# Performance work log

Hardware: AMD Instinct MI355X
Metric: run time of the kernel (lower is better)

## Reference

```python
import jax, jax.numpy as jnp
import numpy as np

GRID_SIZE = 5   # efficient-kan default
K = 3           # spline_order
BATCH = 32768
OBS_DIM = 128
ACTION_DIM = 18
# (in_features, out_features) for the 7 KANLinear layers:
# base: 128->256->256->64 ; adv head: 64->64->18 ; value head: 64->64->1
DIMS = [(OBS_DIM, 256), (256, 256), (256, 64), (64, 64), (64, ACTION_DIM), (64, 64), (64, 1)]


def make_grid(in_f):
    # uniform grid on [-1,1] extended by K knots each side: shape (in_f, GRID_SIZE+2K+1)
    h = 2.0 / GRID_SIZE
    g = jnp.arange(-K, GRID_SIZE + K + 1, dtype=jnp.float32) * h - 1.0
    return jnp.broadcast_to(g, (in_f, g.shape[0]))


def b_splines(x, grid):
    # Cox-de Boor recursion; x: (B, in) -> bases (B, in, GRID_SIZE+K)
    xe = x[:, :, None]
    b = ((xe >= grid[:, :-1]) & (xe < grid[:, 1:])).astype(x.dtype)
    for j in range(1, K + 1):
        left = (xe - grid[:, : -(j + 1)]) / (grid[:, j:-1] - grid[:, : -(j + 1)])
        right = (grid[:, j + 1:] - xe) / (grid[:, j + 1:] - grid[:, 1:-j])
        b = left * b[:, :, :-1] + right * b[:, :, 1:]
    return b


def kan_layer(x, bw, sw, sc):
    # efficient-kan KANLinear: silu base path + spline path with standalone scaler
    grid = make_grid(x.shape[1])
    base = jax.nn.silu(x) @ bw.T                              # (B, out)
    bases = b_splines(x, grid)                                # (B, in, G+K)
    spline = jnp.einsum('big,oig->bo', bases, sw * sc[:, :, None])
    return base + spline


def setup_inputs() -> dict:
    key = jax.random.key(0)
    ks = jax.random.split(key, 1 + 3 * len(DIMS))
    inp = {"x": jax.random.normal(ks[0], (BATCH, OBS_DIM), dtype=jnp.float32)}
    for i, (fin, fout) in enumerate(DIMS):
        inp[f"bw{i}"] = jax.random.normal(ks[1 + 3 * i], (fout, fin), dtype=jnp.float32) / np.sqrt(fin).astype(np.float32)
        inp[f"sw{i}"] = jax.random.normal(ks[2 + 3 * i], (fout, fin, GRID_SIZE + K), dtype=jnp.float32) * (0.1 / np.sqrt(fin).astype(np.float32))
        inp[f"sc{i}"] = 1.0 + 0.1 * jax.random.normal(ks[3 + 3 * i], (fout, fin), dtype=jnp.float32)
    return inp


def reference(x, bw0, sw0, sc0, bw1, sw1, sc1, bw2, sw2, sc2,
              bw3, sw3, sc3, bw4, sw4, sc4, bw5, sw5, sc5, bw6, sw6, sc6):
    h = x
    for bw, sw, sc in [(bw0, sw0, sc0), (bw1, sw1, sc1), (bw2, sw2, sc2)]:
        h = kan_layer(h, bw, sw, sc)
    advantage = kan_layer(kan_layer(h, bw3, sw3, sc3), bw4, sw4, sc4)
    state_value = kan_layer(kan_layer(h, bw5, sw5, sc5), bw6, sw6, sc6)
    return (advantage, state_value)
```

## Files before the change

### kernel.cpp

```cpp
#include <hip/hip_runtime.h>

typedef unsigned short u16;
typedef unsigned int   u32;
typedef unsigned long long u64;
typedef __bf16 bf16;
typedef float f32x4  __attribute__((ext_vector_type(4)));
typedef bf16  bf16x8 __attribute__((ext_vector_type(8)));

__device__ __forceinline__ float bf2f(u16 u){ return (float)__builtin_bit_cast(bf16,u); }
__device__ __forceinline__ u16   f2bf(float f){ return __builtin_bit_cast(u16,(bf16)f); }
__device__ __forceinline__ u32   pkbf(float a,float b){ return (u32)f2bf(a)|((u32)f2bf(b)<<16); }

#define NROWS 32768

__device__ __forceinline__ uint4 basis_pk(float x)
{
  float tp  = __fmaf_rn(x, 2.5f, 5.5f);
  float tpc = fminf(fmaxf(tp, -1.0f), 12.0f);
  float fi  = floorf(tpc);
  float uu  = tpc - fi;
  int   i0  = (int)fi;
  float u2 = uu*uu, u3 = u2*uu, w1 = 1.0f-uu, w2 = w1*w1, w3 = w2*w1;
  float d1 = __fmaf_rn(3.0f, u3, __fmaf_rn(-6.0f, u2, 4.0f));
  float d2 = __fmaf_rn(3.0f, w3, __fmaf_rn(-6.0f, w2, 4.0f));
  u64 dpk = (u64)pkbf(w3, d1) | ((u64)pkbf(d2, u3) << 32);
  int ss = i0*16 - 48;
  u64 A  = dpk << (ss & 63);
  u64 Bv = dpk >> ((64-ss) & 63);
  u64 Cv = dpk << ((ss-64) & 63);
  u64 Dv = dpk >> ((-ss) & 63);
  u64 lo = (ss>=0 && ss<64)   ? A  : ((ss<0 && ss>-64) ? Dv : 0ull);
  u64 hi = (ss>=64 && ss<128) ? Cv : ((ss>0 && ss<64)  ? Bv : 0ull);
  uint4 r; r.x=(u32)lo; r.y=(u32)(lo>>32); r.z=(u32)hi; r.w=(u32)(hi>>32);
  return r;
}

__device__ __forceinline__ void expand9(float x, u16& sil, uint4& bpk)
{
  float s = x * (1.0f/(1.0f+__expf(-x)));
  sil = f2bf(s);
  bpk = basis_pk(x);
}
__device__ __forceinline__ void expand10(float x, u32& spk, uint4& bpk)
{
  float s = x * (1.0f/(1.0f+__expf(-x)));
  u16 uh = f2bf(s);
  u16 ul = f2bf(s - bf2f(uh));
  spk = (u32)uh | ((u32)ul<<16);
  bpk = basis_pk(x);
}

struct PrepArgs {
  const float* bw[7]; const float* sw[7]; const float* sc[7];
  u16* w[7];
  int cin[7]; int coutr[7]; int ntsh[7]; int fmt[7];
  u32 elems[7];
};

__global__ __launch_bounds__(256) void prep_kernel(PrepArgs pa)
{
  u32 idx = blockIdx.x*256 + threadIdx.x;
  int L = 0;
  u32 off = idx;
  while (L < 6 && off >= pa.elems[L]) { off -= pa.elems[L]; ++L; }
  int j    = off & 7;
  int lane = (off>>3) & 63;
  u32 tl   = off >> 9;
  int ntsh = pa.ntsh[L];
  u32 kstep = tl >> ntsh;
  int ntile = (int)(tl & ((1u<<ntsh)-1u));
  int o    = ntile*16 + (lane&15);
  int kpos = (lane>>4)*8 + j;
  int i = 0, g = 0; bool sil;
  if (pa.fmt[L] == 0){
    u32 c = kstep/9u; int r = (int)(kstep - c*9u);
    if (r == 0){ i = (int)c*32 + kpos; sil = true; }
    else { int kl=(r-1)*32+kpos; i=(int)c*32+(kl>>3); g=kl&7; sil = false; }
  } else {
    u32 c = kstep/5u; int r = (int)(kstep - c*5u);
    if (r == 0){ i = (int)c*16 + (kpos>>1); sil = true; }
    else { int kl=(r-1)*32+kpos; i=(int)c*16+(kl>>3); g=kl&7; sil = false; }
  }
  float v = 0.f;
  if (o < pa.coutr[L]) {
    size_t e = (size_t)o*pa.cin[L] + i;
    v = sil ? pa.bw[L][e] : pa.sw[L][e*8+g]*pa.sc[L][e]*0.16666666666666666f;
  }
  pa.w[L][off] = f2bf(v);
}

template<int CIN,int COUT,int IN_MODE,int OUT_MODE>
__global__ __launch_bounds__(512,4) void kan_layer(const void* __restrict__ hin_,
    const u16* __restrict__ W, void* __restrict__ hout_)
{
  constexpr int NCH = CIN/32;
  constexpr int TOTK = NCH*9;
  constexpr int NTILES = COUT/16;
  constexpr int NT = (COUT>=128)? COUT/128 : 1;
  constexpr int SROW=20, BROW=132, BOFF=64*SROW;
  constexpr int CHUNK = BOFF + 64*BROW;
  __shared__ u32 buf[2][CHUNK];

  const int b0 = blockIdx.x*64;
  const int tid = threadIdx.x;
  const int wave = tid>>6, lane = tid&63, m = lane&15, quad = lane>>4;

  const u16*   __restrict__ hb = (const u16*)hin_;
  const float* __restrict__ hf = (const float*)hin_;

  f32x4 acc[4][NT];
#pragma unroll
  for (int a=0;a<4;++a)
#pragma unroll
    for (int n=0;n<NT;++n) acc[a][n]=(f32x4){0.f,0.f,0.f,0.f};

  bf16x8 bbuf[3][NT];
  auto loadB = [&](int kstep, bf16x8* dst){
    if (kstep < TOTK){
#pragma unroll
      for (int nt=0; nt<NT; ++nt)
        dst[nt] = *(const bf16x8*)(W + (((size_t)kstep*NTILES + ((wave*NT+nt)&(NTILES-1)))*64 + lane)*8);
    }
  };
  loadB(0, bbuf[0]); loadB(1, bbuf[1]);

  float xb[2][4];
  auto loadX = [&](int kc, float* dst){
#pragma unroll
    for (int t=0;t<4;++t){
      int task = t*512+tid, row = task>>5, f = task&31;
      int gi = (b0+row)*CIN + kc*32 + f;
      dst[t] = (IN_MODE==0)? hf[gi] : bf2f(hb[gi]);
    }
  };
  auto expandChunk = [&](const float* xc, u32* dstb){
#pragma unroll
    for (int t=0;t<4;++t){
      int task=t*512+tid, row=task>>5, f=task&31;
      u16 sil; uint4 bpk;
      expand9(xc[t], sil, bpk);
      ((u16*)dstb)[row*(SROW*2) + f] = sil;
      *(uint4*)&dstb[BOFF + row*BROW + f*4] = bpk;
    }
  };

  loadX(0, xb[0]);
  expandChunk(xb[0], buf[0]);
  if (NCH > 1) loadX(1, xb[1]);
  __syncthreads();

  for (int kc=0; kc<NCH; ++kc){
    u32* cur = buf[kc&1];
    u32* nxt = buf[(kc+1)&1];
    if (kc+1 < NCH) expandChunk(xb[(kc+1)&1], nxt);
    if (kc+2 < NCH) loadX(kc+2, xb[kc&1]);
#pragma unroll
    for (int ks=0; ks<9; ++ks){
      const int kstep = kc*9 + ks;
      loadB(kstep+2, bbuf[2]);
      bf16x8 af[4];
#pragma unroll
      for (int mt=0; mt<4; ++mt){
        int row = mt*16 + m;
        af[mt] = (ks==0)
          ? *(const bf16x8*)&cur[row*SROW + quad*4]
          : *(const bf16x8*)&cur[BOFF + row*BROW + (ks-1)*16 + quad*4];
      }
#pragma unroll
      for (int nt=0; nt<NT; ++nt)
#pragma unroll
        for (int mt=0; mt<4; ++mt)
          acc[mt][nt] = __builtin_amdgcn_mfma_f32_16x16x32_bf16(af[mt], bbuf[0][nt], acc[mt][nt],0,0,0);
#pragma unroll
      for (int nt=0; nt<NT; ++nt){ bbuf[0][nt]=bbuf[1][nt]; bbuf[1][nt]=bbuf[2][nt]; }
    }
    __syncthreads();
  }

  if (wave*NT < NTILES){
#pragma unroll
    for (int mt=0; mt<4; ++mt)
#pragma unroll
      for (int nt=0; nt<NT; ++nt)
#pragma unroll
        for (int r=0; r<4; ++r){
          size_t off = (size_t)(b0 + mt*16 + quad*4 + r)*COUT + ((wave*NT+nt)&(NTILES-1))*16 + m;
          if constexpr (OUT_MODE==0) ((float*)hout_)[off] = acc[mt][nt][r];
          else                       ((u16*)hout_)[off]   = f2bf(acc[mt][nt][r]);
        }
  }
}

template<int IN_MODE>
__global__ __launch_bounds__(512,4) void tail_kernel(const void* __restrict__ h2_,
  const u16* __restrict__ W3, const u16* __restrict__ W4,
  const u16* __restrict__ W5, const u16* __restrict__ W6,
  float* __restrict__ out_adv, float* __restrict__ out_val)
{
  constexpr int SROW=20, BROW=68, BOFF=64*20;
  __shared__ u32   Aexp[BOFF + 64*BROW];
  __shared__ float hA[64*65], hV[64*65];

  const int b0 = blockIdx.x*64;
  const int tid = threadIdx.x;
  const int wave = tid>>6, lane = tid&63, m = lane&15, quad = lane>>4;
  const int rg = wave>>2, cg = wave&3;

  const u16*   __restrict__ hb = (const u16*)h2_;
  const float* __restrict__ hf = (const float*)h2_;

  f32x4 a3[2], a5[2];
#pragma unroll
  for (int mt=0;mt<2;++mt){ a3[mt]=(f32x4){0,0,0,0}; a5[mt]=(f32x4){0,0,0,0}; }

  bf16x8 w3b[3], w5b[3];
  auto loadB2 = [&](int kstep, int d){
    if (kstep < 20){
      size_t bi = (((size_t)kstep*4 + cg)*64 + lane)*8;
      w3b[d] = *(const bf16x8*)(W3+bi);
      w5b[d] = *(const bf16x8*)(W5+bi);
    }
  };
  loadB2(0,0); loadB2(1,1);

  float xb[2][2];
  auto loadX = [&](int kc, float* dst){
#pragma unroll
    for (int t=0;t<2;++t){
      int task = t*512+tid, row=task>>4, f=task&15;
      int gi = (b0+row)*64 + kc*16 + f;
      dst[t] = (IN_MODE==0)? hf[gi] : bf2f(hb[gi]);
    }
  };
  loadX(0, xb[0]);

  for (int kc=0; kc<4; ++kc){
    const float* xc = xb[kc&1];
#pragma unroll
    for (int t=0;t<2;++t){
      int task=t*512+tid, row=task>>4, f=task&15;
      u32 spk; uint4 bpk;
      expand10(xc[t], spk, bpk);
      Aexp[row*SROW + f] = spk;
      *(uint4*)&Aexp[BOFF + row*BROW + f*4] = bpk;
    }
    if (kc+1 < 4) loadX(kc+1, xb[(kc+1)&1]);
    __syncthreads();
#pragma unroll
    for (int ks=0; ks<5; ++ks){
      const int kstep = kc*5 + ks;
      loadB2(kstep+2, 2);
      bf16x8 af[2];
#pragma unroll
      for (int mt=0; mt<2; ++mt){
        int row = rg*32 + mt*16 + m;
        af[mt] = (ks==0)
          ? *(const bf16x8*)&Aexp[row*SROW + quad*4]
          : *(const bf16x8*)&Aexp[BOFF + row*BROW + (ks-1)*16 + quad*4];
      }
#pragma unroll
      for (int mt=0; mt<2; ++mt){
        a3[mt] = __builtin_amdgcn_mfma_f32_16x16x32_bf16(af[mt], w3b[0], a3[mt],0,0,0);
        a5[mt] = __builtin_amdgcn_mfma_f32_16x16x32_bf16(af[mt], w5b[0], a5[mt],0,0,0);
      }
      w3b[0]=w3b[1]; w3b[1]=w3b[2]; w5b[0]=w5b[1]; w5b[1]=w5b[2];
    }
    __syncthreads();
  }
#pragma unroll
  for (int mt=0;mt<2;++mt)
#pragma unroll
    for (int r=0;r<4;++r){
      int row = rg*32 + mt*16 + quad*4 + r;
      hA[row*65 + cg*16 + m] = a3[mt][r];
      hV[row*65 + cg*16 + m] = a5[mt][r];
    }
  __syncthreads();

  f32x4 a4[2];
#pragma unroll
  for (int mt=0;mt<2;++mt) a4[mt]=(f32x4){0,0,0,0};
  bf16x8 w4b[3];
  auto loadB4 = [&](int kstep, int d){
    if (kstep < 20) w4b[d] = *(const bf16x8*)(W4 + (((size_t)kstep*4 + cg)*64 + lane)*8);
  };
  loadB4(0,0); loadB4(1,1);
  for (int kc=0; kc<4; ++kc){
#pragma unroll
    for (int t=0;t<2;++t){
      int task=t*512+tid, row=task>>4, f=task&15;
      u32 spk; uint4 bpk;
      expand10(hA[row*65 + kc*16 + f], spk, bpk);
      Aexp[row*SROW + f] = spk;
      *(uint4*)&Aexp[BOFF + row*BROW + f*4] = bpk;
    }
    __syncthreads();
#pragma unroll
    for (int ks=0; ks<5; ++ks){
      loadB4(kc*5+ks+2, 2);
      bf16x8 af[2];
#pragma unroll
      for (int mt=0; mt<2; ++mt){
        int row = rg*32 + mt*16 + m;
        af[mt] = (ks==0)
          ? *(const bf16x8*)&Aexp[row*SROW + quad*4]
          : *(const bf16x8*)&Aexp[BOFF + row*BROW + (ks-1)*16 + quad*4];
      }
#pragma unroll
      for (int mt=0; mt<2; ++mt)
        a4[mt] = __builtin_amdgcn_mfma_f32_16x16x32_bf16(af[mt], w4b[0], a4[mt],0,0,0);
      w4b[0]=w4b[1]; w4b[1]=w4b[2];
    }
    __syncthreads();
  }
  {
    int col = cg*16 + m;
    if (col < 18){
#pragma unroll
      for (int mt=0;mt<2;++mt)
#pragma unroll
        for (int r=0;r<4;++r)
          out_adv[(size_t)(b0 + rg*32 + mt*16 + quad*4 + r)*18 + col] = a4[mt][r];
    }
  }

  f32x4 a6[2];
#pragma unroll
  for (int mt=0;mt<2;++mt) a6[mt]=(f32x4){0,0,0,0};
  bf16x8 w6b[3];
  auto loadB6 = [&](int kstep, int d){
    if (kstep < 20) w6b[d] = *(const bf16x8*)(W6 + (((size_t)kstep*4 + cg)*64 + lane)*8);
  };
  loadB6(0,0); loadB6(1,1);
  for (int kc=0; kc<4; ++kc){
#pragma unroll
    for (int t=0;t<2;++t){
      int task=t*512+tid, row=task>>4, f=task&15;
      u32 spk; uint4 bpk;
      expand10(hV[row*65 + kc*16 + f], spk, bpk);
      Aexp[row*SROW + f] = spk;
      *(uint4*)&Aexp[BOFF + row*BROW + f*4] = bpk;
    }
    __syncthreads();
#pragma unroll
    for (int ks=0; ks<5; ++ks){
      loadB6(kc*5+ks+2, 2);
      bf16x8 af[2];
#pragma unroll
      for (int mt=0; mt<2; ++mt){
        int row = rg*32 + mt*16 + m;
        af[mt] = (ks==0)
          ? *(const bf16x8*)&Aexp[row*SROW + quad*4]
          : *(const bf16x8*)&Aexp[BOFF + row*BROW + (ks-1)*16 + quad*4];
      }
#pragma unroll
      for (int mt=0; mt<2; ++mt)
        a6[mt] = __builtin_amdgcn_mfma_f32_16x16x32_bf16(af[mt], w6b[0], a6[mt],0,0,0);
      w6b[0]=w6b[1]; w6b[1]=w6b[2];
    }
    __syncthreads();
  }
  if (cg==0 && m==0){
#pragma unroll
    for (int mt=0;mt<2;++mt)
#pragma unroll
      for (int r=0;r<4;++r)
        out_val[b0 + rg*32 + mt*16 + quad*4 + r] = a6[mt][r];
  }
}

extern "C" void kernel_launch(void* const* d_in, const int* in_sizes, int n_in,
                              void* d_out, int out_size, void* d_ws, size_t ws_size,
                              hipStream_t stream)
{
  (void)in_sizes; (void)n_in; (void)out_size;
  char* ws = (char*)d_ws;

  const size_t wbytes[7] = {589824u, 1179648u, 294912u, 81920u, 81920u, 81920u, 81920u};
  const bool midf32 = ws_size >= 77889536u;

  u16* W[7];
  char *h0, *h1, *h2;
  if (midf32) {
    h0 = ws;
    h1 = h0 + 33554432u;
    h2 = h1 + 33554432u;
    size_t off = 75497472u;
    for (int l=0;l<7;++l){ W[l] = (u16*)(ws+off); off += wbytes[l]; }
  } else {
    h0 = ws;
    h1 = h0 + 16777216u;
    h2 = h1 + 16777216u;
    size_t off = 37748736u;
    for (int l=0;l<7;++l){ W[l] = (u16*)(ws+off); off += wbytes[l]; }
  }

  PrepArgs pa;
  const int cins[7]   = {128,256,256,64,64,64,64};
  const int coutr[7]  = {256,256,64,64,18,64,1};
  const int ntsh[7]   = {4,4,2,2,2,2,2};
  const int fmts[7]   = {0,0,0,1,1,1,1};
  const u32 elems[7]  = {294912u,589824u,147456u,40960u,40960u,40960u,40960u};
  for (int l=0;l<7;++l){
    pa.bw[l] = (const float*)d_in[1+3*l];
    pa.sw[l] = (const float*)d_in[2+3*l];
    pa.sc[l] = (const float*)d_in[3+3*l];
    pa.w[l]  = W[l];
    pa.cin[l]=cins[l]; pa.coutr[l]=coutr[l]; pa.ntsh[l]=ntsh[l]; pa.fmt[l]=fmts[l];
    pa.elems[l]=elems[l];
  }
  prep_kernel<<<4672, 256, 0, stream>>>(pa);

  dim3 g(NROWS/64), b(512);
  float* out_adv = (float*)d_out;
  float* out_val = (float*)d_out + (size_t)NROWS*18;
  if (midf32) {
    kan_layer<128,256,0,0><<<g,b,0,stream>>>(d_in[0], W[0], h0);
    kan_layer<256,256,0,0><<<g,b,0,stream>>>(h0, W[1], h1);
    kan_layer<256, 64,0,0><<<g,b,0,stream>>>(h1, W[2], h2);
    tail_kernel<0><<<g,b,0,stream>>>(h2, W[3], W[4], W[5], W[6], out_adv, out_val);
  } else {
    kan_layer<128,256,0,1><<<g,b,0,stream>>>(d_in[0], W[0], h0);
    kan_layer<256,256,1,1><<<g,b,0,stream>>>(h0, W[1], h1);
    kan_layer<256, 64,1,1><<<g,b,0,stream>>>(h1, W[2], h2);
    tail_kernel<1><<<g,b,0,stream>>>(h2, W[3], W[4], W[5], W[6], out_adv, out_val);
  }
}
```

Baseline: 231.1 us.

## Switch main KAN layers to 32x32x16 MFMA tiles with 256-thread blocks

Rewrites the three main KAN layer kernels to use 32x32x16 bf16 MFMA instructions instead of 16x16x32. Blocks shrink to 4 waves, each computing a larger output fragment, with K-chunks of 16 input features and a deeper B prefetch. The prep kernel repacks the weight layout to match. This aims to reduce LDS A-fragment reads and instruction count per FLOP, at the cost of fewer waves per block, higher register pressure and a changed LDS layout.

Result: slower. 246.9 us (+6.8%).

```diff
diff --git a/kernel.cpp b/kernel.cpp
--- a/kernel.cpp
+++ b/kernel.cpp
@@ -4,8 +4,9 @@
 typedef unsigned int   u32;
 typedef unsigned long long u64;
 typedef __bf16 bf16;
-typedef float f32x4  __attribute__((ext_vector_type(4)));
-typedef bf16  bf16x8 __attribute__((ext_vector_type(8)));
+typedef float f32x4   __attribute__((ext_vector_type(4)));
+typedef float f32x16  __attribute__((ext_vector_type(16)));
+typedef bf16  bf16x8  __attribute__((ext_vector_type(8)));
 
 __device__ __forceinline__ float bf2f(u16 u){ return (float)__builtin_bit_cast(bf16,u); }
 __device__ __forceinline__ u16   f2bf(float f){ return __builtin_bit_cast(u16,(bf16)f); }
@@ -68,15 +69,17 @@
   u32 tl   = off >> 9;
   int ntsh = pa.ntsh[L];
   u32 kstep = tl >> ntsh;
-  int ntile = (int)(tl & ((1u<<ntsh)-1u));
-  int o    = ntile*16 + (lane&15);
-  int kpos = (lane>>4)*8 + j;
-  int i = 0, g = 0; bool sil;
+  int nt   = (int)(tl & ((1u<<ntsh)-1u));
+  int i = 0, g = 0, o; bool sil;
   if (pa.fmt[L] == 0){
+    o = nt*32 + (lane&31);
+    int koct = lane>>5;
     u32 c = kstep/9u; int r = (int)(kstep - c*9u);
-    if (r == 0){ i = (int)c*32 + kpos; sil = true; }
-    else { int kl=(r-1)*32+kpos; i=(int)c*32+(kl>>3); g=kl&7; sil = false; }
+    if (r == 0){ i = (int)c*16 + koct*8 + j; sil = true; }
+    else       { i = (int)c*16 + (r-1)*2 + koct; g = j; sil = false; }
   } else {
+    o = nt*16 + (lane&15);
+    int kpos = (lane>>4)*8 + j;
     u32 c = kstep/5u; int r = (int)(kstep - c*5u);
     if (r == 0){ i = (int)c*16 + (kpos>>1); sil = true; }
     else { int kl=(r-1)*32+kpos; i=(int)c*16+(kl>>3); g=kl&7; sil = false; }
@@ -90,53 +93,58 @@
 }
 
 template<int CIN,int COUT,int IN_MODE,int OUT_MODE>
-__global__ __launch_bounds__(512,4) void kan_layer(const void* __restrict__ hin_,
+__global__ __launch_bounds__(256,2) void kan_layer(const void* __restrict__ hin_,
     const u16* __restrict__ W, void* __restrict__ hout_)
 {
-  constexpr int NCH = CIN/32;
+  constexpr int NCH  = CIN/16;
   constexpr int TOTK = NCH*9;
-  constexpr int NTILES = COUT/16;
-  constexpr int NT = (COUT>=128)? COUT/128 : 1;
-  constexpr int SROW=20, BROW=132, BOFF=64*SROW;
+  constexpr int NT32 = COUT/32;
+  constexpr int RFW  = (COUT>=128)?2:1;
+  constexpr int CFW  = (COUT>=128)?COUT/128:1;
+  constexpr int SROW=12, BROW=68, BOFF=64*SROW;
   constexpr int CHUNK = BOFF + 64*BROW;
   __shared__ u32 buf[2][CHUNK];
 
   const int b0 = blockIdx.x*64;
   const int tid = threadIdx.x;
-  const int wave = tid>>6, lane = tid&63, m = lane&15, quad = lane>>4;
+  const int wave = tid>>6, lane = tid&63, m32 = lane&31, koct = lane>>5;
+  const int rfbase = (COUT>=128)? 0 : (wave>>1);
+  const int cfb    = (COUT>=128)? wave*CFW : (wave&1);
 
   const u16*   __restrict__ hb = (const u16*)hin_;
   const float* __restrict__ hf = (const float*)hin_;
 
-  f32x4 acc[4][NT];
-#pragma unroll
-  for (int a=0;a<4;++a)
-#pragma unroll
-    for (int n=0;n<NT;++n) acc[a][n]=(f32x4){0.f,0.f,0.f,0.f};
-
-  bf16x8 bbuf[3][NT];
+  f32x16 acc[RFW][CFW];
+#pragma unroll
+  for (int a=0;a<RFW;++a)
+#pragma unroll
+    for (int c=0;c<CFW;++c)
+#pragma unroll
+      for (int e=0;e<16;++e) acc[a][c][e] = 0.f;
+
+  bf16x8 bbuf[4][CFW];
   auto loadB = [&](int kstep, bf16x8* dst){
     if (kstep < TOTK){
 #pragma unroll
-      for (int nt=0; nt<NT; ++nt)
-        dst[nt] = *(const bf16x8*)(W + (((size_t)kstep*NTILES + ((wave*NT+nt)&(NTILES-1)))*64 + lane)*8);
-    }
-  };
-  loadB(0, bbuf[0]); loadB(1, bbuf[1]);
+      for (int cf=0; cf<CFW; ++cf)
+        dst[cf] = *(const bf16x8*)(W + (((size_t)kstep*NT32 + cfb+cf)*64 + lane)*8);
+    }
+  };
+  loadB(0, bbuf[0]); loadB(1, bbuf[1]); loadB(2, bbuf[2]);
 
   float xb[2][4];
   auto loadX = [&](int kc, float* dst){
 #pragma unroll
     for (int t=0;t<4;++t){
-      int task = t*512+tid, row = task>>5, f = task&31;
-      int gi = (b0+row)*CIN + kc*32 + f;
+      int task = t*256+tid, row = task>>4, f = task&15;
+      int gi = (b0+row)*CIN + kc*16 + f;
       dst[t] = (IN_MODE==0)? hf[gi] : bf2f(hb[gi]);
     }
   };
   auto expandChunk = [&](const float* xc, u32* dstb){
 #pragma unroll
     for (int t=0;t<4;++t){
-      int task=t*512+tid, row=task>>5, f=task&31;
+      int task=t*256+tid, row=task>>4, f=task&15;
       u16 sil; uint4 bpk;
       expand9(xc[t], sil, bpk);
       ((u16*)dstb)[row*(SROW*2) + f] = sil;
@@ -157,38 +165,37 @@
 #pragma unroll
     for (int ks=0; ks<9; ++ks){
       const int kstep = kc*9 + ks;
-      loadB(kstep+2, bbuf[2]);
-      bf16x8 af[4];
-#pragma unroll
-      for (int mt=0; mt<4; ++mt){
-        int row = mt*16 + m;
-        af[mt] = (ks==0)
-          ? *(const bf16x8*)&cur[row*SROW + quad*4]
-          : *(const bf16x8*)&cur[BOFF + row*BROW + (ks-1)*16 + quad*4];
-      }
-#pragma unroll
-      for (int nt=0; nt<NT; ++nt)
-#pragma unroll
-        for (int mt=0; mt<4; ++mt)
-          acc[mt][nt] = __builtin_amdgcn_mfma_f32_16x16x32_bf16(af[mt], bbuf[0][nt], acc[mt][nt],0,0,0);
-#pragma unroll
-      for (int nt=0; nt<NT; ++nt){ bbuf[0][nt]=bbuf[1][nt]; bbuf[1][nt]=bbuf[2][nt]; }
-    }
-    __syncthreads();
-  }
-
-  if (wave*NT < NTILES){
-#pragma unroll
-    for (int mt=0; mt<4; ++mt)
-#pragma unroll
-      for (int nt=0; nt<NT; ++nt)
-#pragma unroll
-        for (int r=0; r<4; ++r){
-          size_t off = (size_t)(b0 + mt*16 + quad*4 + r)*COUT + ((wave*NT+nt)&(NTILES-1))*16 + m;
-          if constexpr (OUT_MODE==0) ((float*)hout_)[off] = acc[mt][nt][r];
-          else                       ((u16*)hout_)[off]   = f2bf(acc[mt][nt][r]);
-        }
-  }
+      loadB(kstep+3, bbuf[3]);
+      bf16x8 af[RFW];
+#pragma unroll
+      for (int rf=0; rf<RFW; ++rf){
+        int row = (rfbase+rf)*32 + m32;
+        af[rf] = (ks==0)
+          ? *(const bf16x8*)&cur[row*SROW + koct*4]
+          : *(const bf16x8*)&cur[BOFF + row*BROW + (ks-1)*8 + koct*4];
+      }
+#pragma unroll
+      for (int cf=0; cf<CFW; ++cf)
+#pragma unroll
+        for (int rf=0; rf<RFW; ++rf)
+          acc[rf][cf] = __builtin_amdgcn_mfma_f32_32x32x16_bf16(af[rf], bbuf[0][cf], acc[rf][cf],0,0,0);
+#pragma unroll
+      for (int cf=0; cf<CFW; ++cf){ bbuf[0][cf]=bbuf[1][cf]; bbuf[1][cf]=bbuf[2][cf]; bbuf[2][cf]=bbuf[3][cf]; }
+    }
+    __syncthreads();
+  }
+
+#pragma unroll
+  for (int rf=0; rf<RFW; ++rf)
+#pragma unroll
+    for (int cf=0; cf<CFW; ++cf)
+#pragma unroll
+      for (int reg=0; reg<16; ++reg){
+        int rl  = (reg&3) + 8*(reg>>2) + 4*koct;
+        size_t off = (size_t)(b0 + (rfbase+rf)*32 + rl)*COUT + (cfb+cf)*32 + m32;
+        if constexpr (OUT_MODE==0) ((float*)hout_)[off] = acc[rf][cf][reg];
+        else                       ((u16*)hout_)[off]   = f2bf(acc[rf][cf][reg]);
+      }
 }
 
 template<int IN_MODE>
@@ -398,7 +405,7 @@
   PrepArgs pa;
   const int cins[7]   = {128,256,256,64,64,64,64};
   const int coutr[7]  = {256,256,64,64,18,64,1};
-  const int ntsh[7]   = {4,4,2,2,2,2,2};
+  const int ntsh[7]   = {3,3,1,2,2,2,2};
   const int fmts[7]   = {0,0,0,1,1,1,1};
   const u32 elems[7]  = {294912u,589824u,147456u,40960u,40960u,40960u,40960u};
   for (int l=0;l<7;++l){
@@ -411,18 +418,18 @@
   }
   prep_kernel<<<4672, 256, 0, stream>>>(pa);
 
-  dim3 g(NROWS/64), b(512);
+  dim3 g(NROWS/64), bmain(256), btail(512);
   float* out_adv = (float*)d_out;
   float* out_val = (float*)d_out + (size_t)NROWS*18;
   if (midf32) {
-    kan_layer<128,256,0,0><<<g,b,0,stream>>>(d_in[0], W[0], h0);
-    kan_layer<256,256,0,0><<<g,b,0,stream>>>(h0, W[1], h1);
-    kan_layer<256, 64,0,0><<<g,b,0,stream>>>(h1, W[2], h2);
-    tail_kernel<0><<<g,b,0,stream>>>(h2, W[3], W[4], W[5], W[6], out_adv, out_val);
+    kan_layer<128,256,0,0><<<g,bmain,0,stream>>>(d_in[0], W[0], h0);
+    kan_layer<256,256,0,0><<<g,bmain,0,stream>>>(h0, W[1], h1);
+    kan_layer<256, 64,0,0><<<g,bmain,0,stream>>>(h1, W[2], h2);
+    tail_kernel<0><<<g,btail,0,stream>>>(h2, W[3], W[4], W[5], W[6], out_adv, out_val);
   } else {
-    kan_layer<128,256,0,1><<<g,b,0,stream>>>(d_in[0], W[0], h0);
-    kan_layer<256,256,1,1><<<g,b,0,stream>>>(h0, W[1], h1);
-    kan_layer<256, 64,1,1><<<g,b,0,stream>>>(h1, W[2], h2);
-    tail_kernel<1><<<g,b,0,stream>>>(h2, W[3], W[4], W[5], W[6], out_adv, out_val);
-  }
-}
+    kan_layer<128,256,0,1><<<g,bmain,0,stream>>>(d_in[0], W[0], h0);
+    kan_layer<256,256,1,1><<<g,bmain,0,stream>>>(h0, W[1], h1);
+    kan_layer<256, 64,1,1><<<g,bmain,0,stream>>>(h1, W[2], h2);
+    tail_kernel<1><<<g,btail,0,stream>>>(h2, W[3], W[4], W[5], W[6], out_adv, out_val);
+  }
+}
```
